# Performance work log

Measured on AMD Instinct MI355X. Metric: run time of the kernel, lower is better.

## Reference

```python
import jax, jax.numpy as jnp
import numpy as np

N, E, B = 100000, 800000, 64
IN, HC1, HC2, NC, SA = 256, 128, 32, 2, 350
NEG = 0.2  # GATv2Conv default negative_slope


def forward(s_x, s_edge_index, s_batch, s_root_n_id,
            Wq, bq, Wk, bk, Wv, bv,
            Wl1, bl1, Wr1, br1, att1, bias1,
            Wl2, bl2, Wr2, br2, att2, bias2,
            Wl3, bl3, Wr3, br3, att3, bias3,
            c1w, c1b, c2W, c2b, c3W, c3b,
            linW, linb, aW1, ab1, aW2, mW1, mb1, mW2, mb2):
    src, dst = s_edge_index[0], s_edge_index[1]
    x_info = s_x
    # --- SelfAttention over seq_len=1 (x.unsqueeze(1)) ---
    z = s_x[:, None, :]                                   # [N,1,IN]
    q = z @ Wq + bq; k = z @ Wk + bk; v = z @ Wv + bv      # [N,1,SA]
    scores = jnp.einsum('nqd,nkd->nqk', q, k) / jnp.sqrt(jnp.float32(SA))
    probs = jax.nn.softmax(scores, axis=-1)
    h = jnp.einsum('nqk,nkd->nqd', probs, v)[:, 0, :]      # [N,SA]

    def gatv2(x, Wl, bl, Wr, br, att, bias):
        # PyG GATv2Conv, heads=1, eval mode (dropout off)
        xl = x @ Wl + bl                                   # source transform [N,O]
        xr = x @ Wr + br                                   # target transform [N,O]
        e = jax.nn.leaky_relu(xl[src] + xr[dst], NEG)      # [E,O]
        s = e @ att                                        # [E]
        smax = jax.ops.segment_max(s, dst, num_segments=N)
        smax = jnp.where(jnp.isfinite(smax), smax, 0.0)
        ex = jnp.exp(s - smax[dst])
        den = jax.ops.segment_sum(ex, dst, num_segments=N)
        alpha = ex / jnp.maximum(den[dst], 1e-16)
        return jax.ops.segment_sum(alpha[:, None] * xl[src], dst, num_segments=N) + bias

    h = jax.nn.relu(gatv2(h, Wl1, bl1, Wr1, br1, att1, bias1))
    h = jax.nn.relu(gatv2(h, Wl2, bl2, Wr2, br2, att2, bias2))
    h = jax.nn.relu(gatv2(h, Wl3, bl3, Wr3, br3, att3, bias3))   # [N,HC2]

    # --- readout: root node feature ++ global mean pool ---
    cnt = jax.ops.segment_sum(jnp.ones((N,), h.dtype), s_batch, num_segments=B)
    pooled = jax.ops.segment_sum(h, s_batch, num_segments=B) / jnp.maximum(cnt, 1.0)[:, None]
    sx = jnp.concatenate([h[s_root_n_id], pooled], axis=-1)       # [B,2*HC2]

    # --- info branch on raw root features ---
    info = x_info[s_root_n_id]                                    # [B,IN]
    info = c1w[0] * info[:, :-2] + c1w[1] * info[:, 1:-1] + c1w[2] * info[:, 2:] + c1b  # Conv1d(1,1,3)
    t = info.T                                                    # [IN-2,B]
    t = jax.nn.relu(c2W @ t + c2b[:, None])                       # [HC1,B]
    t = jax.nn.relu(c3W @ t + c3b[:, None])                       # [HC1//2,B]
    t = t.T                                                       # [B,HC1//2]
    L = t.shape[1]
    t = jax.nn.relu(t.reshape(B, HC2, L // HC2).mean(-1))         # AdaptiveAvgPool1d(HC2)

    sx = jax.nn.relu(sx @ linW + linb)                            # [B,HC2]

    # --- semantic attention over the two views ---
    emb = jnp.stack([sx, t], axis=1)                              # [B,2,HC2]
    w = jnp.tanh(emb @ aW1 + ab1) @ aW2                           # [B,2,1]
    beta = jax.nn.softmax(w, axis=1)
    emb = (beta * emb).sum(1)                                     # [B,HC2]

    return jax.nn.softmax(jnp.tanh(emb @ mW1 + mb1) @ mW2 + mb2, axis=1)  # [B,NC]


def setup_inputs() -> dict:
    keys = iter(jax.random.split(jax.random.key(0), 64))
    def nrm(*shape):
        return jax.random.normal(next(keys), shape, dtype=jnp.float32) * 0.05
    inp = {}
    inp['s_x'] = jax.random.normal(next(keys), (N, IN), dtype=jnp.float32)
    inp['s_edge_index'] = jax.random.randint(next(keys), (2, E), 0, N)
    inp['s_batch'] = jnp.sort(jax.random.randint(next(keys), (N,), 0, B))
    inp['s_root_n_id'] = jax.random.randint(next(keys), (B,), 0, N)
    inp['Wq'] = nrm(IN, SA); inp['bq'] = nrm(SA)
    inp['Wk'] = nrm(IN, SA); inp['bk'] = nrm(SA)
    inp['Wv'] = nrm(IN, SA); inp['bv'] = nrm(SA)
    inp['Wl1'] = nrm(SA, HC1); inp['bl1'] = nrm(HC1)
    inp['Wr1'] = nrm(SA, HC1); inp['br1'] = nrm(HC1)
    inp['att1'] = nrm(HC1); inp['bias1'] = nrm(HC1)
    inp['Wl2'] = nrm(HC1, HC1 // 2); inp['bl2'] = nrm(HC1 // 2)
    inp['Wr2'] = nrm(HC1, HC1 // 2); inp['br2'] = nrm(HC1 // 2)
    inp['att2'] = nrm(HC1 // 2); inp['bias2'] = nrm(HC1 // 2)
    inp['Wl3'] = nrm(HC1 // 2, HC2); inp['bl3'] = nrm(HC2)
    inp['Wr3'] = nrm(HC1 // 2, HC2); inp['br3'] = nrm(HC2)
    inp['att3'] = nrm(HC2); inp['bias3'] = nrm(HC2)
    inp['c1w'] = nrm(3); inp['c1b'] = nrm(1)
    inp['c2W'] = nrm(HC1, IN - 2); inp['c2b'] = nrm(HC1)
    inp['c3W'] = nrm(HC1 // 2, HC1); inp['c3b'] = nrm(HC1 // 2)
    inp['linW'] = nrm(2 * HC2, HC2); inp['linb'] = nrm(HC2)
    inp['aW1'] = nrm(HC2, 16); inp['ab1'] = nrm(16); inp['aW2'] = nrm(16, 1)
    inp['mW1'] = nrm(HC2, 16); inp['mb1'] = nrm(16)
    inp['mW2'] = nrm(16, NC); inp['mb2'] = nrm(NC)
    return inp


def reference(s_x, s_edge_index, s_batch, s_root_n_id,
              Wq, bq, Wk, bk, Wv, bv,
              Wl1, bl1, Wr1, br1, att1, bias1,
              Wl2, bl2, Wr2, br2, att2, bias2,
              Wl3, bl3, Wr3, br3, att3, bias3,
              c1w, c1b, c2W, c2b, c3W, c3b,
              linW, linb, aW1, ab1, aW2, mW1, mb1, mW2, mb2):
    return forward(s_x, s_edge_index, s_batch, s_root_n_id,
                   Wq, bq, Wk, bk, Wv, bv,
                   Wl1, bl1, Wr1, br1, att1, bias1,
                   Wl2, bl2, Wr2, br2, att2, bias2,
                   Wl3, bl3, Wr3, br3, att3, bias3,
                   c1w, c1b, c2W, c2b, c3W, c3b,
                   linW, linb, aW1, ab1, aW2, mW1, mb1, mW2, mb2)
```

## Files before the change

kernel.cpp:

```cpp
#include <hip/hip_runtime.h>
#include <hip/hip_bf16.h>
#include <math.h>

typedef unsigned short ushort_t;
typedef __attribute__((ext_vector_type(8))) short bfrag;
typedef __attribute__((ext_vector_type(4))) float ffrag;

#define GLOBAL_AS __attribute__((address_space(1)))
#define LDS_AS    __attribute__((address_space(3)))

constexpr int N_NODES = 100000;
constexpr int N_EDGES = 800000;
constexpr int NB      = 64;
constexpr int IN_F    = 256;
constexpr int HC1C    = 128;
constexpr int HC2C    = 32;
constexpr int SA_D    = 350;
constexpr float NEG   = 0.2f;

constexpr int SCAN_NBLK = (N_NODES + 255) / 256;
constexpr int MB64      = (N_NODES + 63) / 64;

constexpr size_t OFF_WT1    = 0;
constexpr size_t OFF_WT2    = OFF_WT1 + 65536;
constexpr size_t OFF_WT3    = OFF_WT2 + 16384;
constexpr size_t OFF_BC1    = OFF_WT3 + 4096;
constexpr size_t OFF_BC2    = OFF_BC1 + 256;
constexpr size_t OFF_BC3    = OFF_BC2 + 128;
constexpr size_t OFF_XLR    = OFF_BC3 + 64;
constexpr size_t OFF_H      = OFF_XLR + (size_t)N_NODES * 256;
constexpr size_t OFF_DEG    = OFF_H + (size_t)N_NODES * 128;
constexpr size_t OFF_ROWPTR = OFF_DEG + N_NODES;
constexpr size_t OFF_CURSOR = OFF_ROWPTR + N_NODES + 1;
constexpr size_t OFF_BLKS   = OFF_CURSOR + N_NODES;
constexpr size_t OFF_BLKO   = OFF_BLKS + 512;
constexpr size_t OFF_CSRSRC = OFF_BLKO + 512;
constexpr size_t OFF_POOLED = OFF_CSRSRC + N_EDGES;
constexpr size_t OFF_CNT    = OFF_POOLED + NB * HC2C;
constexpr size_t WS_FLOATS  = OFF_CNT + NB;

__device__ __forceinline__ ushort_t f2bf(float f) {
  union { float f; unsigned int u; } a;
  a.f = f;
  unsigned int r = a.u + 0x7FFFu + ((a.u >> 16) & 1u);
  return (ushort_t)(r >> 16);
}
__device__ __forceinline__ float bf2f(ushort_t h) {
  union { unsigned int u; float f; } a;
  a.u = ((unsigned int)h) << 16;
  return a.f;
}
__device__ __forceinline__ float2 bfp(unsigned int u) {
  float2 r;
  r.x = __uint_as_float(u << 16);
  r.y = __uint_as_float(u & 0xFFFF0000u);
  return r;
}
__device__ __forceinline__ unsigned int pack2(float a, float b) {
  unsigned int ua = __float_as_uint(a);
  ua += 0x7FFFu + ((ua >> 16) & 1u);
  unsigned int ub = __float_as_uint(b);
  ub += 0x7FFFu + ((ub >> 16) & 1u);
  return __builtin_amdgcn_perm(ub, ua, 0x07060302u);
}
__device__ __forceinline__ void unp8(uint4 u, float* x) {
  float2 p0 = bfp(u.x), p1 = bfp(u.y), p2 = bfp(u.z), p3 = bfp(u.w);
  x[0] = p0.x; x[1] = p0.y; x[2] = p1.x; x[3] = p1.y;
  x[4] = p2.x; x[5] = p2.y; x[6] = p3.x; x[7] = p3.y;
}

__global__ void k_pack_all(const float* __restrict__ Wv, const float* __restrict__ bv,
                           const float* __restrict__ Wl1, const float* __restrict__ bl1,
                           const float* __restrict__ Wr1, const float* __restrict__ br1,
                           const float* __restrict__ Wl2, const float* __restrict__ bl2,
                           const float* __restrict__ Wr2, const float* __restrict__ br2,
                           const float* __restrict__ Wl3, const float* __restrict__ bl3,
                           const float* __restrict__ Wr3, const float* __restrict__ br3,
                           ushort_t* __restrict__ WT1, float* __restrict__ bc1,
                           ushort_t* __restrict__ WT2, float* __restrict__ bc2,
                           ushort_t* __restrict__ WT3, float* __restrict__ bc3) {
  int blk = blockIdx.x;
  int tid = threadIdx.x;
  if (blk < 256) {
    int t = blk * 256 + tid;
    int n = t & 255, k = t >> 8;
    const float* Wx = (n < 128) ? Wl1 : Wr1;
    int j = n & 127;
    float a = 0.f;
    for (int kk = 0; kk < SA_D; ++kk) a += Wv[k * SA_D + kk] * Wx[kk * 128 + j];
    WT1[(size_t)n * 256 + k] = f2bf(a);
  } else if (blk == 256) {
    int n = tid;
    const float* Wx = (n < 128) ? Wl1 : Wr1;
    const float* bx = (n < 128) ? bl1 : br1;
    int j = n & 127;
    float a = bx[j];
    for (int kk = 0; kk < SA_D; ++kk) a += bv[kk] * Wx[kk * 128 + j];
    bc1[n] = a;
  } else if (blk < 321) {
    int t = (blk - 257) * 256 + tid;
    int n = t & 127, k = t >> 7;
    if (t < 128) bc2[t] = (t < 64) ? bl2[t] : br2[t - 64];
    float v = (n < 64) ? Wl2[k * 64 + n] : Wr2[k * 64 + (n - 64)];
    WT2[(size_t)n * 128 + k] = f2bf(v);
  } else {
    int t = (blk - 321) * 256 + tid;
    int n = t & 63, k = t >> 6;
    if (t < 64) bc3[t] = (t < 32) ? bl3[t] : br3[t - 32];
    float v = (n < 32) ? Wl3[k * 32 + n] : Wr3[k * 32 + (n - 32)];
    WT3[(size_t)n * 64 + k] = f2bf(v);
  }
}

__global__ void k_hist(const int* __restrict__ dst, int* __restrict__ deg) {
  int e = blockIdx.x * blockDim.x + threadIdx.x;
  if (e < N_EDGES) atomicAdd(deg + dst[e], 1);
}

__global__ void k_scan_local(const int* __restrict__ deg, int* __restrict__ row_ptr,
                             int* __restrict__ blk_sum) {
  __shared__ int sh[256];
  int t = threadIdx.x;
  int i = blockIdx.x * 256 + t;
  int v = (i < N_NODES) ? deg[i] : 0;
  sh[t] = v;
  __syncthreads();
  for (int off = 1; off < 256; off <<= 1) {
    int add = (t >= off) ? sh[t - off] : 0;
    __syncthreads();
    sh[t] += add;
    __syncthreads();
  }
  if (i < N_NODES) row_ptr[i] = sh[t] - v;
  if (t == 255) blk_sum[blockIdx.x] = sh[255];
}

__global__ void k_scan_blk(const int* __restrict__ blk_sum, int* __restrict__ blk_off) {
  __shared__ int sh[512];
  int t = threadIdx.x;
  int v = (t < SCAN_NBLK) ? blk_sum[t] : 0;
  sh[t] = v;
  __syncthreads();
  for (int off = 1; off < 512; off <<= 1) {
    int add = (t >= off) ? sh[t - off] : 0;
    __syncthreads();
    sh[t] += add;
    __syncthreads();
  }
  blk_off[t] = sh[t] - v;
}

__global__ void k_scan_add(int* __restrict__ row_ptr, const int* __restrict__ blk_off,
                           int* __restrict__ cursor) {
  int i = blockIdx.x * blockDim.x + threadIdx.x;
  if (i < N_NODES) {
    int v = row_ptr[i] + blk_off[i >> 8];
    row_ptr[i] = v;
    cursor[i] = v;
  }
  if (i == 0) row_ptr[N_NODES] = N_EDGES;
}

__global__ void k_fill(const int* __restrict__ src, const int* __restrict__ dst,
                       int* __restrict__ cursor, int* __restrict__ csr_src) {
  int e = blockIdx.x * blockDim.x + threadIdx.x;
  if (e >= N_EDGES) return;
  int pos = atomicAdd(cursor + dst[e], 1);
  csr_src[pos] = src[e];
}

template <int K, int NN, int BN, bool AF32>
__global__ __launch_bounds__(256, 4) void k_gemm_bf16(const void* __restrict__ xin,
                                                      const ushort_t* __restrict__ WT,
                                                      const float* __restrict__ bc,
                                                      ushort_t* __restrict__ out, int M) {
  constexpr int RT  = 2;
  constexpr int CT  = BN / 32;
  constexpr int NK  = K / 32;
  constexpr int BGI = (BN * 32 * 2 / 16) / 256;
  constexpr int BUS = 2048 + BN * 32;
  __shared__ __align__(16) ushort_t lds[2][BUS];

  const int tid  = threadIdx.x;
  const int wave = tid >> 6;
  const int lane = tid & 63;
  const int quad = lane >> 4;
  const int l16  = lane & 15;
  const int wrow = wave >> 1;
  const int wcol = wave & 1;
  const int m0   = blockIdx.x * 64;
  const int n0   = blockIdx.y * BN;

  const float*    af32 = (const float*)xin;
  const ushort_t* ab16 = (const ushort_t*)xin;

  const int aline = tid >> 3, alg = tid & 7;
  const int arow  = aline * 2 + (alg >> 2);
  int am = m0 + arow;
  if (am >= M) am = M - 1;
  const size_t aoff = (size_t)am * K + (alg & 3) * 8;
  const int awi = aline * 64 + ((alg ^ (aline & 7)) * 8);
  const int ainner = (tid & 7) ^ (aline & 7);
  const int arow2  = aline * 2 + (ainner >> 2);
  int am2 = m0 + arow2;
  if (am2 >= M) am2 = M - 1;
  const size_t aoff2 = (size_t)am2 * K + (ainner & 3) * 8;

  size_t boff[BGI];
#pragma unroll
  for (int g = 0; g < BGI; ++g) {
    const int s = g * 256 + tid;
    const int bline  = s >> 3;
    const int binner = (s & 7) ^ (bline & 7);
    const int brow   = bline * 2 + (binner >> 2);
    boff[g] = (size_t)(n0 + brow) * K + (binner & 3) * 8;
  }

  int ard[RT];
#pragma unroll
  for (int rt = 0; rt < RT; ++rt) {
    const int row = wrow * 32 + rt * 16 + l16;
    const int line = row >> 1;
    ard[rt] = line * 64 + ((((row & 1) * 4 + quad) ^ (line & 7)) * 8);
  }
  int brd[CT];
#pragma unroll
  for (int ct = 0; ct < CT; ++ct) {
    const int rowb = wcol * (BN / 2) + ct * 16 + l16;
    const int lineb = rowb >> 1;
    brd[ct] = 2048 + lineb * 64 + ((((rowb & 1) * 4 + quad) ^ (lineb & 7)) * 8);
  }

  float4 af0, af1;

#define ALOAD(ks)                                                          \
  do {                                                                     \
    af0 = *(const float4*)(af32 + aoff + (size_t)(ks) * 32);               \
    af1 = *(const float4*)(af32 + aoff + (size_t)(ks) * 32 + 4);           \
  } while (0)

#define APACK(BUF)                                                         \
  do {                                                                     \
    uint4 w;                                                               \
    w.x = pack2(af0.x, af0.y);                                             \
    w.y = pack2(af0.z, af0.w);                                             \
    w.z = pack2(af1.x, af1.y);                                             \
    w.w = pack2(af1.z, af1.w);                                             \
    *(uint4*)&lds[BUF][awi] = w;                                           \
  } while (0)

#define STAGE_A_GL(ks, BUF)                                                \
  __builtin_amdgcn_global_load_lds(                                        \
      (const GLOBAL_AS unsigned int*)(ab16 + aoff2 + (size_t)(ks) * 32),   \
      (LDS_AS unsigned int*)&lds[BUF][(size_t)(wave * 64) * 8], 16, 0, 0)

#define STAGE_B(ks, BUF)                                                   \
  do {                                                                     \
    _Pragma("unroll")                                                      \
    for (int g = 0; g < BGI; ++g)                                          \
      __builtin_amdgcn_global_load_lds(                                    \
          (const GLOBAL_AS unsigned int*)(WT + boff[g] + (size_t)(ks) * 32), \
          (LDS_AS unsigned int*)&lds[BUF][2048 + (size_t)((g * 256 + wave * 64) * 8)], \
          16, 0, 0);                                                       \
  } while (0)

#define KSTEP(BUF)                                                         \
  do {                                                                     \
    bfrag a0 = *(const bfrag*)&lds[BUF][ard[0]];                           \
    bfrag a1 = *(const bfrag*)&lds[BUF][ard[1]];                           \
    _Pragma("unroll")                                                      \
    for (int ct = 0; ct < CT; ++ct) {                                      \
      bfrag bf = *(const bfrag*)&lds[BUF][brd[ct]];                        \
      acc[0][ct] = __builtin_amdgcn_mfma_f32_16x16x32_bf16(a0, bf, acc[0][ct], 0, 0, 0); \
      acc[1][ct] = __builtin_amdgcn_mfma_f32_16x16x32_bf16(a1, bf, acc[1][ct], 0, 0, 0); \
    }                                                                      \
  } while (0)

  ffrag acc[RT][CT];
#pragma unroll
  for (int rt = 0; rt < RT; ++rt)
#pragma unroll
    for (int ct = 0; ct < CT; ++ct) acc[rt][ct] = ffrag{0.f, 0.f, 0.f, 0.f};

  if constexpr (AF32) {
    ALOAD(0);
    STAGE_B(0, 0);
    APACK(0);
  } else {
    STAGE_A_GL(0, 0);
    STAGE_B(0, 0);
  }
  __syncthreads();

#pragma unroll
  for (int i = 0; i < NK; ++i) {
    const int cur = i & 1;
    if (i + 1 < NK) {
      if constexpr (AF32) ALOAD(i + 1);
      else                STAGE_A_GL(i + 1, cur ^ 1);
      STAGE_B(i + 1, cur ^ 1);
    }
    KSTEP(cur);
    if (i + 1 < NK) {
      if constexpr (AF32) APACK(cur ^ 1);
      __syncthreads();
    }
  }
#undef ALOAD
#undef APACK
#undef STAGE_A_GL
#undef STAGE_B
#undef KSTEP

#pragma unroll
  for (int rt = 0; rt < RT; ++rt)
#pragma unroll
    for (int ct = 0; ct < CT; ++ct) {
      const int n = n0 + wcol * (BN / 2) + ct * 16 + l16;
      const float bb = bc[n];
#pragma unroll
      for (int r = 0; r < 4; ++r) {
        const int m = m0 + wrow * 32 + rt * 16 + quad * 4 + r;
        if (m < M) out[(size_t)m * NN + n] = f2bf(acc[rt][ct][r] + bb);
      }
    }
}

template <int C>
__global__ void k_gat(const ushort_t* __restrict__ xlr, const int* __restrict__ row_ptr,
                      const int* __restrict__ csr_src, const float* __restrict__ att,
                      const float* __restrict__ bias, ushort_t* __restrict__ h) {
  constexpr int G = C / 8;
  constexpr int RS = 2 * C;
  int t = blockIdx.x * blockDim.x + threadIdx.x;
  int d = t / G;
  int lane = t - d * G;
  if (d >= N_NODES) return;
  float xr[8], a[8];
  unp8(*(const uint4*)(xlr + (size_t)d * RS + C + lane * 8), xr);
  *(float4*)&a[0] = *(const float4*)(att + lane * 8);
  *(float4*)&a[4] = *(const float4*)(att + lane * 8 + 4);
  float acc[8];
#pragma unroll
  for (int j = 0; j < 8; ++j) acc[j] = 0.f;
  float den = 0.f;
  const int e0 = row_ptr[d], e1 = row_ptr[d + 1];
  int i = e0;
  for (; i + 4 <= e1; i += 4) {
    uint4 u[4];
#pragma unroll
    for (int q = 0; q < 4; ++q)
      u[q] = *(const uint4*)(xlr + (size_t)csr_src[i + q] * RS + lane * 8);
    float xl[4][8];
#pragma unroll
    for (int q = 0; q < 4; ++q) unp8(u[q], xl[q]);
    float p[4] = {0.f, 0.f, 0.f, 0.f};
#pragma unroll
    for (int j = 0; j < 8; ++j) {
#pragma unroll
      for (int q = 0; q < 4; ++q) {
        float v = xl[q][j] + xr[j];
        v = v > 0.f ? v : NEG * v;
        p[q] += a[j] * v;
      }
    }
#pragma unroll
    for (int off = G / 2; off > 0; off >>= 1) {
#pragma unroll
      for (int q = 0; q < 4; ++q) p[q] += __shfl_xor(p[q], off, 64);
    }
    float ex[4];
#pragma unroll
    for (int q = 0; q < 4; ++q) ex[q] = expf(p[q]);
    den += (ex[0] + ex[1]) + (ex[2] + ex[3]);
#pragma unroll
    for (int j = 0; j < 8; ++j)
      acc[j] += (ex[0] * xl[0][j] + ex[1] * xl[1][j]) + (ex[2] * xl[2][j] + ex[3] * xl[3][j]);
  }
  for (; i < e1; ++i) {
    int s = csr_src[i];
    float xl[8];
    unp8(*(const uint4*)(xlr + (size_t)s * RS + lane * 8), xl);
    float p = 0.f;
#pragma unroll
    for (int j = 0; j < 8; ++j) {
      float v = xl[j] + xr[j];
      v = v > 0.f ? v : NEG * v;
      p += a[j] * v;
    }
#pragma unroll
    for (int off = G / 2; off > 0; off >>= 1) p += __shfl_xor(p, off, 64);
    float ex = expf(p);
    den += ex;
#pragma unroll
    for (int j = 0; j < 8; ++j) acc[j] += ex * xl[j];
  }
  float inv = 1.f / fmaxf(den, 1e-16f);
  float o[8];
#pragma unroll
  for (int j = 0; j < 8; ++j)
    o[j] = fmaxf(acc[j] * inv + bias[lane * 8 + j], 0.f);
  uint4 pk;
  pk.x = pack2(o[0], o[1]);
  pk.y = pack2(o[2], o[3]);
  pk.z = pack2(o[4], o[5]);
  pk.w = pack2(o[6], o[7]);
  *(uint4*)(h + (size_t)d * C + lane * 8) = pk;
}

__global__ void k_pool(const ushort_t* __restrict__ h3, const int* __restrict__ batch,
                       float* __restrict__ pooled, float* __restrict__ cnt) {
  constexpr int NPB = 1024;
  constexpr int NPT = NPB / 8;
  int c = threadIdx.x & 31;
  int r = threadIdx.x >> 5;
  int base = blockIdx.x * NPB + r * NPT;
  if (base >= N_NODES) return;
  int end = base + NPT;
  if (end > N_NODES) end = N_NODES;
  int cur_b = batch[base];
  float acc = 0.f, count = 0.f;
  for (int n = base; n < end; ++n) {
    int b = batch[n];
    if (b != cur_b) {
      atomicAdd(pooled + cur_b * HC2C + c, acc);
      if (c == 0) atomicAdd(cnt + cur_b, count);
      cur_b = b;
      acc = 0.f;
      count = 0.f;
    }
    acc += bf2f(h3[(size_t)n * HC2C + c]);
    count += 1.f;
  }
  atomicAdd(pooled + cur_b * HC2C + c, acc);
  if (c == 0) atomicAdd(cnt + cur_b, count);
}

__global__ __launch_bounds__(256) void k_tail(
    const ushort_t* __restrict__ h3, const int* __restrict__ root,
    const float* __restrict__ pooled, const float* __restrict__ cnt,
    const float* __restrict__ linW, const float* __restrict__ linb,
    const float* __restrict__ X, const float* __restrict__ c1w,
    const float* __restrict__ c1b, const float* __restrict__ c2W,
    const float* __restrict__ c2b, const float* __restrict__ c3W,
    const float* __restrict__ c3b, const float* __restrict__ aW1,
    const float* __restrict__ ab1, const float* __restrict__ aW2,
    const float* __restrict__ mW1, const float* __restrict__ mb1,
    const float* __restrict__ mW2, const float* __restrict__ mb2,
    float* __restrict__ out) {
  constexpr int L = IN_F - 2;
  __shared__ float s_info[L];
  __shared__ float s_t1[HC1C];
  __shared__ float s_t2[HC1C / 2];
  __shared__ float s_e0[HC2C];
  __shared__ float s_e1[HC2C];
  const int b = blockIdx.x;
  const int tid = threadIdx.x;
  const int r = root[b];
  const float* xr = X + (size_t)r * IN_F;
  for (int i = tid; i < L; i += 256)
    s_info[i] = c1w[0] * xr[i] + c1w[1] * xr[i + 1] + c1w[2] * xr[i + 2] + c1b[0];
  __syncthreads();
  if (tid < HC1C) {
    float a = c2b[tid];
    for (int i = 0; i < L; ++i) a += c2W[tid * L + i] * s_info[i];
    s_t1[tid] = fmaxf(a, 0.f);
  }
  __syncthreads();
  if (tid < HC1C / 2) {
    float a = c3b[tid];
    for (int i = 0; i < HC1C; ++i) a += c3W[tid * HC1C + i] * s_t1[i];
    s_t2[tid] = fmaxf(a, 0.f);
  }
  __syncthreads();
  if (tid < HC2C) {
    float v = 0.5f * (s_t2[2 * tid] + s_t2[2 * tid + 1]);
    s_e1[tid] = fmaxf(v, 0.f);
  } else if (tid < 2 * HC2C) {
    int j = tid - HC2C;
    float inv = 1.f / fmaxf(cnt[b], 1.f);
    float a = linb[j];
    for (int c = 0; c < HC2C; ++c) a += bf2f(h3[(size_t)r * HC2C + c]) * linW[c * HC2C + j];
    for (int c = 0; c < HC2C; ++c) a += pooled[b * HC2C + c] * inv * linW[(HC2C + c) * HC2C + j];
    s_e0[j] = fmaxf(a, 0.f);
  }
  __syncthreads();
  if (tid == 0) {
    float w0 = 0.f, w1 = 0.f;
    for (int j = 0; j < 16; ++j) {
      float z0 = ab1[j], z1 = ab1[j];
      for (int c = 0; c < HC2C; ++c) {
        z0 += s_e0[c] * aW1[c * 16 + j];
        z1 += s_e1[c] * aW1[c * 16 + j];
      }
      w0 += tanhf(z0) * aW2[j];
      w1 += tanhf(z1) * aW2[j];
    }
    float mx = fmaxf(w0, w1);
    float x0 = expf(w0 - mx), x1 = expf(w1 - mx);
    float inv = 1.f / (x0 + x1);
    float b0 = x0 * inv, b1 = x1 * inv;
    float l0 = mb2[0], l1 = mb2[1];
    for (int j = 0; j < 16; ++j) {
      float z = mb1[j];
      for (int c = 0; c < HC2C; ++c) z += (b0 * s_e0[c] + b1 * s_e1[c]) * mW1[c * 16 + j];
      float tz = tanhf(z);
      l0 += tz * mW2[j * 2 + 0];
      l1 += tz * mW2[j * 2 + 1];
    }
    float m2 = fmaxf(l0, l1);
    float y0 = expf(l0 - m2), y1 = expf(l1 - m2);
    float is = 1.f / (y0 + y1);
    out[b * 2 + 0] = y0 * is;
    out[b * 2 + 1] = y1 * is;
  }
}

extern "C" void kernel_launch(void* const* d_in, const int* in_sizes, int n_in, void* d_out,
                              int out_size, void* d_ws, size_t ws_size, hipStream_t stream) {
  if (ws_size < WS_FLOATS * sizeof(float)) return;

  const float* s_x   = (const float*)d_in[0];
  const int*   edge  = (const int*)d_in[1];
  const int*   batch = (const int*)d_in[2];
  const int*   root  = (const int*)d_in[3];
  const float* Wv    = (const float*)d_in[8];
  const float* bv    = (const float*)d_in[9];
  const float* Wl1   = (const float*)d_in[10];
  const float* bl1   = (const float*)d_in[11];
  const float* Wr1   = (const float*)d_in[12];
  const float* br1   = (const float*)d_in[13];
  const float* att1  = (const float*)d_in[14];
  const float* bias1 = (const float*)d_in[15];
  const float* Wl2   = (const float*)d_in[16];
  const float* bl2   = (const float*)d_in[17];
  const float* Wr2   = (const float*)d_in[18];
  const float* br2   = (const float*)d_in[19];
  const float* att2  = (const float*)d_in[20];
  const float* bias2 = (const float*)d_in[21];
  const float* Wl3   = (const float*)d_in[22];
  const float* bl3   = (const float*)d_in[23];
  const float* Wr3   = (const float*)d_in[24];
  const float* br3   = (const float*)d_in[25];
  const float* att3  = (const float*)d_in[26];
  const float* bias3 = (const float*)d_in[27];
  const float* c1w   = (const float*)d_in[28];
  const float* c1b   = (const float*)d_in[29];
  const float* c2W   = (const float*)d_in[30];
  const float* c2b   = (const float*)d_in[31];
  const float* c3W   = (const float*)d_in[32];
  const float* c3b   = (const float*)d_in[33];
  const float* linW  = (const float*)d_in[34];
  const float* linb  = (const float*)d_in[35];
  const float* aW1   = (const float*)d_in[36];
  const float* ab1   = (const float*)d_in[37];
  const float* aW2   = (const float*)d_in[38];
  const float* mW1   = (const float*)d_in[39];
  const float* mb1   = (const float*)d_in[40];
  const float* mW2   = (const float*)d_in[41];
  const float* mb2   = (const float*)d_in[42];

  const int* src = edge;
  const int* dst = edge + N_EDGES;

  float*    ws      = (float*)d_ws;
  ushort_t* WT1     = (ushort_t*)(ws + OFF_WT1);
  ushort_t* WT2     = (ushort_t*)(ws + OFF_WT2);
  ushort_t* WT3     = (ushort_t*)(ws + OFF_WT3);
  float*    bc1     = ws + OFF_BC1;
  float*    bc2     = ws + OFF_BC2;
  float*    bc3     = ws + OFF_BC3;
  ushort_t* xlr     = (ushort_t*)(ws + OFF_XLR);
  ushort_t* hbuf    = (ushort_t*)(ws + OFF_H);
  int*      deg     = (int*)(ws + OFF_DEG);
  int*      row_ptr = (int*)(ws + OFF_ROWPTR);
  int*      cursor  = (int*)(ws + OFF_CURSOR);
  int*      blks    = (int*)(ws + OFF_BLKS);
  int*      blko    = (int*)(ws + OFF_BLKO);
  int*      csr_src = (int*)(ws + OFF_CSRSRC);
  float*    pooled  = ws + OFF_POOLED;
  float*    cnt     = ws + OFF_CNT;
  float*    out     = (float*)d_out;

  hipMemsetAsync(deg, 0, N_NODES * sizeof(int), stream);
  k_hist<<<(N_EDGES + 255) / 256, 256, 0, stream>>>(dst, deg);
  k_scan_local<<<SCAN_NBLK, 256, 0, stream>>>(deg, row_ptr, blks);
  k_scan_blk<<<1, 512, 0, stream>>>(blks, blko);
  k_scan_add<<<SCAN_NBLK, 256, 0, stream>>>(row_ptr, blko, cursor);
  k_fill<<<(N_EDGES + 255) / 256, 256, 0, stream>>>(src, dst, cursor, csr_src);

  k_pack_all<<<337, 256, 0, stream>>>(Wv, bv, Wl1, bl1, Wr1, br1, Wl2, bl2, Wr2, br2, Wl3,
                                      bl3, Wr3, br3, WT1, bc1, WT2, bc2, WT3, bc3);

  k_gemm_bf16<256, 256, 128, true><<<dim3(MB64, 2), 256, 0, stream>>>(s_x, WT1, bc1, xlr,
                                                                      N_NODES);
  k_gat<128><<<(N_NODES * 16 + 255) / 256, 256, 0, stream>>>(xlr, row_ptr, csr_src, att1,
                                                             bias1, hbuf);

  k_gemm_bf16<128, 128, 128, false><<<dim3(MB64, 1), 256, 0, stream>>>(hbuf, WT2, bc2, xlr,
                                                                       N_NODES);
  k_gat<64><<<(N_NODES * 8 + 255) / 256, 256, 0, stream>>>(xlr, row_ptr, csr_src, att2,
                                                           bias2, hbuf);

  k_gemm_bf16<64, 64, 64, false><<<dim3(MB64, 1), 256, 0, stream>>>(hbuf, WT3, bc3, xlr,
                                                                    N_NODES);
  k_gat<32><<<(N_NODES * 4 + 255) / 256, 256, 0, stream>>>(xlr, row_ptr, csr_src, att3,
                                                           bias3, hbuf);

  hipMemsetAsync(pooled, 0, (NB * HC2C + NB) * sizeof(float), stream);
  k_pool<<<(N_NODES + 1023) / 1024, 256, 0, stream>>>(hbuf, batch, pooled, cnt);
  k_tail<<<NB, 256, 0, stream>>>(hbuf, root, pooled, cnt, linW, linb, s_x, c1w, c1b, c2W,
                                 c2b, c3W, c3b, aW1, ab1, aW2, mW1, mb1, mW2, mb2, out);
}
```

Baseline: 624.6 us.

## Fuse histogram into weight packing and fold mean-pool into tail kernel

Merges the edge in-degree histogram into the weight-packing kernel as extra blocks, and removes the separate pooling kernel and its memset. The tail kernel now binary-searches the batch array for each graph's node range and sums that graph's features with 8 warps. This cuts two launches and a memset, but it assumes the batch array is sorted. Each tail block now scans its own graph serially with only 64 blocks, which may be slower than the parallel pool.

New measurement: 624.6 us. Within noise of the previous version (-0.0%).

```diff
diff --git a/kernel.cpp b/kernel.cpp
--- a/kernel.cpp
+++ b/kernel.cpp
@@ -18,8 +18,10 @@
 constexpr int SA_D    = 350;
 constexpr float NEG   = 0.2f;
 
-constexpr int SCAN_NBLK = (N_NODES + 255) / 256;
-constexpr int MB64      = (N_NODES + 63) / 64;
+constexpr int SCAN_NBLK  = (N_NODES + 255) / 256;
+constexpr int MB64       = (N_NODES + 63) / 64;
+constexpr int PACK_BLKS  = 337;
+constexpr int HIST_BLKS  = (N_EDGES + 255) / 256;
 
 constexpr size_t OFF_WT1    = 0;
 constexpr size_t OFF_WT2    = OFF_WT1 + 65536;
@@ -69,18 +71,24 @@
   x[4] = p2.x; x[5] = p2.y; x[6] = p3.x; x[7] = p3.y;
 }
 
-__global__ void k_pack_all(const float* __restrict__ Wv, const float* __restrict__ bv,
-                           const float* __restrict__ Wl1, const float* __restrict__ bl1,
-                           const float* __restrict__ Wr1, const float* __restrict__ br1,
-                           const float* __restrict__ Wl2, const float* __restrict__ bl2,
-                           const float* __restrict__ Wr2, const float* __restrict__ br2,
-                           const float* __restrict__ Wl3, const float* __restrict__ bl3,
-                           const float* __restrict__ Wr3, const float* __restrict__ br3,
-                           ushort_t* __restrict__ WT1, float* __restrict__ bc1,
-                           ushort_t* __restrict__ WT2, float* __restrict__ bc2,
-                           ushort_t* __restrict__ WT3, float* __restrict__ bc3) {
+__global__ void k_hist_pack(const int* __restrict__ dst, int* __restrict__ deg,
+                            const float* __restrict__ Wv, const float* __restrict__ bv,
+                            const float* __restrict__ Wl1, const float* __restrict__ bl1,
+                            const float* __restrict__ Wr1, const float* __restrict__ br1,
+                            const float* __restrict__ Wl2, const float* __restrict__ bl2,
+                            const float* __restrict__ Wr2, const float* __restrict__ br2,
+                            const float* __restrict__ Wl3, const float* __restrict__ bl3,
+                            const float* __restrict__ Wr3, const float* __restrict__ br3,
+                            ushort_t* __restrict__ WT1, float* __restrict__ bc1,
+                            ushort_t* __restrict__ WT2, float* __restrict__ bc2,
+                            ushort_t* __restrict__ WT3, float* __restrict__ bc3) {
   int blk = blockIdx.x;
   int tid = threadIdx.x;
+  if (blk >= PACK_BLKS) {
+    int e = (blk - PACK_BLKS) * 256 + tid;
+    if (e < N_EDGES) atomicAdd(deg + dst[e], 1);
+    return;
+  }
   if (blk < 256) {
     int t = blk * 256 + tid;
     int n = t & 255, k = t >> 8;
@@ -112,11 +120,6 @@
   }
 }
 
-__global__ void k_hist(const int* __restrict__ dst, int* __restrict__ deg) {
-  int e = blockIdx.x * blockDim.x + threadIdx.x;
-  if (e < N_EDGES) atomicAdd(deg + dst[e], 1);
-}
-
 __global__ void k_scan_local(const int* __restrict__ deg, int* __restrict__ row_ptr,
                              int* __restrict__ blk_sum) {
   __shared__ int sh[256];
@@ -408,37 +411,9 @@
   *(uint4*)(h + (size_t)d * C + lane * 8) = pk;
 }
 
-__global__ void k_pool(const ushort_t* __restrict__ h3, const int* __restrict__ batch,
-                       float* __restrict__ pooled, float* __restrict__ cnt) {
-  constexpr int NPB = 1024;
-  constexpr int NPT = NPB / 8;
-  int c = threadIdx.x & 31;
-  int r = threadIdx.x >> 5;
-  int base = blockIdx.x * NPB + r * NPT;
-  if (base >= N_NODES) return;
-  int end = base + NPT;
-  if (end > N_NODES) end = N_NODES;
-  int cur_b = batch[base];
-  float acc = 0.f, count = 0.f;
-  for (int n = base; n < end; ++n) {
-    int b = batch[n];
-    if (b != cur_b) {
-      atomicAdd(pooled + cur_b * HC2C + c, acc);
-      if (c == 0) atomicAdd(cnt + cur_b, count);
-      cur_b = b;
-      acc = 0.f;
-      count = 0.f;
-    }
-    acc += bf2f(h3[(size_t)n * HC2C + c]);
-    count += 1.f;
-  }
-  atomicAdd(pooled + cur_b * HC2C + c, acc);
-  if (c == 0) atomicAdd(cnt + cur_b, count);
-}
-
 __global__ __launch_bounds__(256) void k_tail(
     const ushort_t* __restrict__ h3, const int* __restrict__ root,
-    const float* __restrict__ pooled, const float* __restrict__ cnt,
+    const int* __restrict__ batch,
     const float* __restrict__ linW, const float* __restrict__ linb,
     const float* __restrict__ X, const float* __restrict__ c1w,
     const float* __restrict__ c1b, const float* __restrict__ c2W,
@@ -454,13 +429,32 @@
   __shared__ float s_t2[HC1C / 2];
   __shared__ float s_e0[HC2C];
   __shared__ float s_e1[HC2C];
+  __shared__ float s_part[8][HC2C];
+  __shared__ float s_pool[HC2C];
+  __shared__ int   s_lohi[2];
   const int b = blockIdx.x;
   const int tid = threadIdx.x;
   const int r = root[b];
   const float* xr = X + (size_t)r * IN_F;
   for (int i = tid; i < L; i += 256)
     s_info[i] = c1w[0] * xr[i] + c1w[1] * xr[i + 1] + c1w[2] * xr[i + 2] + c1b[0];
+  if (tid == 0) {
+    int lo = 0, hi = N_NODES;
+    while (lo < hi) { int m = (lo + hi) >> 1; if (batch[m] < b) lo = m + 1; else hi = m; }
+    s_lohi[0] = lo;
+    int lo2 = lo, hi2 = N_NODES;
+    while (lo2 < hi2) { int m = (lo2 + hi2) >> 1; if (batch[m] <= b) lo2 = m + 1; else hi2 = m; }
+    s_lohi[1] = lo2;
+  }
   __syncthreads();
+  const int lo = s_lohi[0], hi = s_lohi[1];
+  {
+    const int c = tid & 31, rr = tid >> 5;
+    float pa = 0.f;
+    for (int i = lo + rr; i < hi; i += 8)
+      pa += bf2f(h3[(size_t)i * HC2C + c]);
+    s_part[rr][c] = pa;
+  }
   if (tid < HC1C) {
     float a = c2b[tid];
     for (int i = 0; i < L; ++i) a += c2W[tid * L + i] * s_info[i];
@@ -471,6 +465,12 @@
     float a = c3b[tid];
     for (int i = 0; i < HC1C; ++i) a += c3W[tid * HC1C + i] * s_t1[i];
     s_t2[tid] = fmaxf(a, 0.f);
+  } else if (tid < HC1C / 2 + HC2C) {
+    const int cc = tid - HC1C / 2;
+    float s = 0.f;
+#pragma unroll
+    for (int rr = 0; rr < 8; ++rr) s += s_part[rr][cc];
+    s_pool[cc] = s;
   }
   __syncthreads();
   if (tid < HC2C) {
@@ -478,10 +478,10 @@
     s_e1[tid] = fmaxf(v, 0.f);
   } else if (tid < 2 * HC2C) {
     int j = tid - HC2C;
-    float inv = 1.f / fmaxf(cnt[b], 1.f);
+    float inv = 1.f / fmaxf((float)(hi - lo), 1.f);
     float a = linb[j];
     for (int c = 0; c < HC2C; ++c) a += bf2f(h3[(size_t)r * HC2C + c]) * linW[c * HC2C + j];
-    for (int c = 0; c < HC2C; ++c) a += pooled[b * HC2C + c] * inv * linW[(HC2C + c) * HC2C + j];
+    for (int c = 0; c < HC2C; ++c) a += s_pool[c] * inv * linW[(HC2C + c) * HC2C + j];
     s_e0[j] = fmaxf(a, 0.f);
   }
   __syncthreads();
@@ -578,20 +578,18 @@
   int*      blks    = (int*)(ws + OFF_BLKS);
   int*      blko    = (int*)(ws + OFF_BLKO);
   int*      csr_src = (int*)(ws + OFF_CSRSRC);
-  float*    pooled  = ws + OFF_POOLED;
-  float*    cnt     = ws + OFF_CNT;
   float*    out     = (float*)d_out;
 
   hipMemsetAsync(deg, 0, N_NODES * sizeof(int), stream);
-  k_hist<<<(N_EDGES + 255) / 256, 256, 0, stream>>>(dst, deg);
+  k_hist_pack<<<PACK_BLKS + HIST_BLKS, 256, 0, stream>>>(
+      dst, deg, Wv, bv, Wl1, bl1, Wr1, br1, Wl2, bl2, Wr2, br2, Wl3, bl3, Wr3, br3,
+      WT1, bc1, WT2, bc2, WT3, bc3);
+
   k_scan_local<<<SCAN_NBLK, 256, 0, stream>>>(deg, row_ptr, blks);
   k_scan_blk<<<1, 512, 0, stream>>>(blks, blko);
   k_scan_add<<<SCAN_NBLK, 256, 0, stream>>>(row_ptr, blko, cursor);
   k_fill<<<(N_EDGES + 255) / 256, 256, 0, stream>>>(src, dst, cursor, csr_src);
 
-  k_pack_all<<<337, 256, 0, stream>>>(Wv, bv, Wl1, bl1, Wr1, br1, Wl2, bl2, Wr2, br2, Wl3,
-                                      bl3, Wr3, br3, WT1, bc1, WT2, bc2, WT3, bc3);
-
   k_gemm_bf16<256, 256, 128, true><<<dim3(MB64, 2), 256, 0, stream>>>(s_x, WT1, bc1, xlr,
                                                                       N_NODES);
   k_gat<128><<<(N_NODES * 16 + 255) / 256, 256, 0, stream>>>(xlr, row_ptr, csr_src, att1,
@@ -607,8 +605,6 @@
   k_gat<32><<<(N_NODES * 4 + 255) / 256, 256, 0, stream>>>(xlr, row_ptr, csr_src, att3,
                                                            bias3, hbuf);
 
-  hipMemsetAsync(pooled, 0, (NB * HC2C + NB) * sizeof(float), stream);
-  k_pool<<<(N_NODES + 1023) / 1024, 256, 0, stream>>>(hbuf, batch, pooled, cnt);
-  k_tail<<<NB, 256, 0, stream>>>(hbuf, root, pooled, cnt, linW, linb, s_x, c1w, c1b, c2W,
+  k_tail<<<NB, 256, 0, stream>>>(hbuf, root, batch, linW, linb, s_x, c1w, c1b, c2W,
                                  c2b, c3W, c3b, aW1, ab1, aW2, mW1, mb1, mW2, mb2, out);
 }
```
